# Performance work log

Hardware: AMD Instinct MI355X
Metric: run time of the kernel (lower is better)

## Reference

```python
import jax, jax.numpy as jnp
import numpy as np

B, L, D_MODEL = 2, 2048, 1024
EXPAND, D_STATE, D_CONV = 2, 16, 4
D_INNER = EXPAND * D_MODEL          # 2048
DT_RANK = D_MODEL // 16             # 64 (mamba-ssm 'auto' rank)


def setup_inputs() -> dict:
    key = jax.random.key(0)
    ks = jax.random.split(key, 8)
    s = lambda k, shape, scale: jax.random.normal(k, shape, jnp.float32) * scale
    x = s(ks[0], (B, L, D_MODEL), 1.0)
    W_in = s(ks[1], (2 * D_INNER, D_MODEL), D_MODEL ** -0.5)
    conv_w = s(ks[2], (D_INNER, 1, D_CONV), D_CONV ** -0.5)   # depthwise kernel
    conv_b = s(ks[3], (D_INNER,), 0.02)
    W_xproj = s(ks[4], (DT_RANK + 2 * D_STATE, D_INNER), D_INNER ** -0.5)
    W_dt = s(ks[5], (D_INNER, DT_RANK), DT_RANK ** -0.5)
    # inverse-softplus of dt ~= 0.01 (mamba default dt init region)
    b_dt = jnp.log(jnp.expm1(0.01 * jnp.ones((D_INNER,), jnp.float32)))
    # S4D-real init: A = -[1..d_state] per channel
    A_log = jnp.log(jnp.broadcast_to(
        jnp.arange(1, D_STATE + 1, dtype=jnp.float32), (D_INNER, D_STATE)))
    D = jnp.ones((D_INNER,), jnp.float32)
    W_out = s(ks[6], (D_MODEL, D_INNER), D_INNER ** -0.5)
    return dict(x=x, W_in=W_in, conv_w=conv_w, conv_b=conv_b, W_xproj=W_xproj,
                W_dt=W_dt, b_dt=b_dt, A_log=A_log, D=D, W_out=W_out)


def reference(x, W_in, conv_w, conv_b, W_xproj, W_dt, b_dt, A_log, D, W_out):
    # in_proj: [B,L,d_model] -> [B,L,2*d_inner]
    xz = jnp.einsum('bld,ed->ble', x, W_in)
    xs, z = jnp.split(xz, 2, axis=-1)

    # causal depthwise conv1d over time, kernel d_conv
    xc = jnp.swapaxes(xs, 1, 2)  # [B, d_inner, L]
    xc = jax.lax.conv_general_dilated(
        xc, conv_w, window_strides=(1,), padding=[(D_CONV - 1, 0)],
        feature_group_count=D_INNER)
    xc = xc + conv_b[None, :, None]
    xs = jax.nn.silu(jnp.swapaxes(xc, 1, 2))  # [B,L,d_inner]

    # x_proj -> (dt, B, C)
    x_dbl = jnp.einsum('bld,ed->ble', xs, W_xproj)
    dt, Bm, Cm = jnp.split(x_dbl, [DT_RANK, DT_RANK + D_STATE], axis=-1)
    dt = jax.nn.softplus(jnp.einsum('blr,dr->bld', dt, W_dt) + b_dt)  # [B,L,d_inner]

    A = -jnp.exp(A_log)  # [d_inner, d_state]

    def step(h, inp):
        dt_t, B_t, C_t, x_t = inp  # [B,d], [B,n], [B,n], [B,d]
        dA = jnp.exp(dt_t[..., None] * A)                       # [B,d,n]
        h = h * dA + (dt_t * x_t)[..., None] * B_t[:, None, :]  # [B,d,n]
        y = jnp.einsum('bdn,bn->bd', h, C_t)
        return h, y

    tm = lambda a: jnp.swapaxes(a, 0, 1)  # time-major for scan
    h0 = jnp.zeros((x.shape[0], D_INNER, D_STATE), x.dtype)
    _, ys = jax.lax.scan(step, h0, (tm(dt), tm(Bm), tm(Cm), tm(xs)))

    y = tm(ys) + xs * D          # skip term D*x
    y = y * jax.nn.silu(z)       # gate
    return jnp.einsum('bld,ed->ble', y, W_out)  # out_proj -> [B,L,d_model]
```

## Files before the change

kernel.cpp:

```cpp
#include <hip/hip_runtime.h>
#include <cstdint>
#include <cstddef>

typedef __bf16 bf16_t;
typedef bf16_t bf16x4 __attribute__((ext_vector_type(4)));
typedef bf16_t bf16x8 __attribute__((ext_vector_type(8)));
typedef float f32x4 __attribute__((ext_vector_type(4)));

static __device__ __forceinline__ void glds16(const void* g, void* l) {
    __builtin_amdgcn_global_load_lds((const __attribute__((address_space(1))) void*)g,
                                     (__attribute__((address_space(3))) void*)l,
                                     16, 0, 0);
}

#define BARRIER()  asm volatile("s_barrier" ::: "memory")
#define DS_WAIT()  do { asm volatile("s_waitcnt lgkmcnt(0)" ::: "memory"); \
                        __builtin_amdgcn_sched_barrier(0); } while (0)

__global__ __launch_bounds__(256)
void cast5(const float* __restrict__ s0, bf16_t* __restrict__ d0, int n0,
           const float* __restrict__ s1, bf16_t* __restrict__ d1, int n1,
           const float* __restrict__ s2, bf16_t* __restrict__ d2, int n2,
           const float* __restrict__ s3, bf16_t* __restrict__ d3, int n3,
           const float* __restrict__ s4, bf16_t* __restrict__ d4)
{
    int bb = blockIdx.x;
    const float* s; bf16_t* d;
    if (bb < n0)              { s = s0; d = d0; }
    else if ((bb -= n0) < n1) { s = s1; d = d1; }
    else if ((bb -= n1) < n2) { s = s2; d = d2; }
    else if ((bb -= n2) < n3) { s = s3; d = d3; }
    else                      { bb -= n3; s = s4; d = d4; }
    const size_t base = (size_t)bb * 1024 + threadIdx.x * 4;
    const f32x4 v = *(const f32x4*)(s + base);
    bf16x4 o;
    o[0] = (bf16_t)v[0]; o[1] = (bf16_t)v[1]; o[2] = (bf16_t)v[2]; o[3] = (bf16_t)v[3];
    *(bf16x4*)(d + base) = o;
}

#define LOAD_A(MQ) \
    _Pragma("unroll") for (int mf = 0; mf < 4; ++mf) { \
        aF[mf][0] = *(const bf16x8*)(Ab + (aRow + (MQ)*64 + mf*16)*64 + ck0); \
        aF[mf][1] = *(const bf16x8*)(Ab + (aRow + (MQ)*64 + mf*16)*64 + ck1); }

#define LOAD_B(NQ, dst) \
    _Pragma("unroll") for (int nf = 0; nf < 2; ++nf) { \
        dst[nf][0] = *(const bf16x8*)(Bb + (bRow + (NQ)*32 + nf*16)*64 + ck0); \
        dst[nf][1] = *(const bf16x8*)(Bb + (bRow + (NQ)*32 + nf*16)*64 + ck1); }

#define MFMA16(MQ, NQ, bset) \
    __builtin_amdgcn_s_setprio(1); \
    _Pragma("unroll") for (int mf = 0; mf < 4; ++mf) \
    _Pragma("unroll") for (int nf = 0; nf < 2; ++nf) \
    _Pragma("unroll") for (int kk = 0; kk < 2; ++kk) \
        acc[(MQ)*4+mf][(NQ)*2+nf] = __builtin_amdgcn_mfma_f32_16x16x32_bf16( \
            aF[mf][kk], bset[nf][kk], acc[(MQ)*4+mf][(NQ)*2+nf], 0, 0, 0); \
    __builtin_amdgcn_s_setprio(0);

template<int EPI, int SPLITK>
__global__ __launch_bounds__(512, 2)
void gemm256_bt(const bf16_t* __restrict__ A, const bf16_t* __restrict__ Bt,
                const int N, const int K, const int KC,
                bf16_t* __restrict__ o0, bf16_t* __restrict__ o1,
                float* __restrict__ p0, float* __restrict__ p1,
                float* __restrict__ p2, float* __restrict__ p3)
{
    constexpr int TILE = 256 * 64;
    __shared__ __align__(16) bf16_t As[2 * TILE];
    __shared__ __align__(16) bf16_t Bs[2 * TILE];

    const int tid  = threadIdx.x;
    const int lane = tid & 63;
    const int w    = tid >> 6;
    const int wm   = w >> 2, wn = w & 3;
    const int l16  = lane & 15, quad = lane >> 4;
    const int e7   = l16 & 7;
    const int ck0  = (quad ^ e7) << 3;
    const int ck1  = ck0 ^ 32;
    const int lr   = lane >> 3, l8 = lane & 7;
    const int swz  = (l8 ^ lr) << 3;
    const int m0   = blockIdx.y * 256, n0 = blockIdx.x * 256;
    const int z    = (SPLITK > 1) ? blockIdx.z : 0;
    const int NT   = KC >> 6;

    if (SPLITK > 1) { A += (size_t)z * KC; Bt += (size_t)z * KC; }

    const int aRow = wm * 128 + l16;
    const int bRow = wn * 64 + l16;

    f32x4 acc[8][4] = {};
    bf16x8 aF[4][2], bLo[2][2], bHi[2][2];

    auto STAGE = [&](int unit, int kt, int d) {
        const bf16_t* g; int rg0; bf16_t* lb; int rbase;
        if (unit <= 1) { g = A;  rg0 = m0; lb = As;
                         rbase = unit * 64 + w * 8; }
        else           { g = Bt; rg0 = n0; lb = Bs;
                         rbase = ((w >> 2) << 6) + ((w & 3) << 3) + ((unit & 1) << 5); }
#pragma unroll
        for (int L = 0; L < 2; ++L) {
            const int rb = rbase + L * 128;
            glds16(g + (size_t)(rg0 + rb + lr) * K + kt * 64 + swz,
                   lb + d * TILE + rb * 64);
        }
    };

    STAGE(2, 0, 0); STAGE(0, 0, 0); STAGE(3, 0, 0); STAGE(1, 0, 0);
    if (NT > 1) { STAGE(2, 1, 1); STAGE(0, 1, 1); STAGE(3, 1, 1); }
    if (NT > 1) asm volatile("s_waitcnt vmcnt(6)" ::: "memory");
    else        asm volatile("s_waitcnt vmcnt(0)" ::: "memory");
    BARRIER();

    for (int i = 0; i < NT; ++i) {
        const int b = i & 1;
        const bf16_t* Ab = As + b * TILE;
        const bf16_t* Bb = Bs + b * TILE;

        LOAD_A(0); LOAD_B(0, bLo);
        if (i + 1 < NT) STAGE(1, i + 1, (i + 1) & 1);
        BARRIER(); DS_WAIT();
        MFMA16(0, 0, bLo);
        __builtin_amdgcn_sched_barrier(0);
        BARRIER();

        LOAD_B(1, bHi);
        if (i + 2 < NT) STAGE(2, i + 2, b);
        BARRIER(); DS_WAIT();
        MFMA16(0, 1, bHi);
        __builtin_amdgcn_sched_barrier(0);
        BARRIER();

        LOAD_A(1);
        if (i + 2 < NT) { STAGE(0, i + 2, b); STAGE(3, i + 2, b); }
        BARRIER(); DS_WAIT();
        MFMA16(1, 1, bHi);
        MFMA16(1, 0, bLo);
        __builtin_amdgcn_sched_barrier(0);
        if (i + 2 < NT) asm volatile("s_waitcnt vmcnt(6)" ::: "memory");
        else            asm volatile("s_waitcnt vmcnt(0)" ::: "memory");
        BARRIER();
    }

    float* pz = (EPI == 3) ? ((z == 0) ? p0 : (z == 1) ? p1 : (z == 2) ? p2 : p3)
                           : nullptr;
#pragma unroll
    for (int mf = 0; mf < 8; ++mf)
#pragma unroll
        for (int nf = 0; nf < 4; ++nf)
#pragma unroll
            for (int r = 0; r < 4; ++r) {
                const int gr = m0 + wm * 128 + mf * 16 + quad * 4 + r;
                const int gc = n0 + wn * 64 + nf * 16 + l16;
                const float v = acc[mf][nf][r];
                if (EPI == 1) {
                    if (gc < 2048) o0[(size_t)gr * 2048 + gc] = (bf16_t)v;
                    else           o1[(size_t)gr * 2048 + (gc - 2048)] = (bf16_t)v;
                } else if (EPI == 3) {
                    pz[(size_t)gr * N + gc] = v;
                } else {
                    ((float*)o0)[(size_t)gr * N + gc] = v;
                }
            }
}

template<int EPI, int SPLITK>
__global__ __launch_bounds__(256)
void gemm_bt(const bf16_t* __restrict__ A, const bf16_t* __restrict__ Bt,
             const int M, const int N, const int K,
             void* __restrict__ o0, void* __restrict__ o1,
             const float* __restrict__ bias,
             float* __restrict__ p0, float* __restrict__ p1,
             float* __restrict__ p2, float* __restrict__ p3)
{
    __shared__ __align__(16) bf16_t As[128 * 64];
    __shared__ __align__(16) bf16_t Bs[128 * 64];

    const int tid  = threadIdx.x;
    const int lane = tid & 63;
    const int wave = tid >> 6;
    const int wm = wave & 1, wn = wave >> 1;
    const int m0 = blockIdx.y * 128, n0 = blockIdx.x * 128;
    const int quad = lane >> 4, l16 = lane & 15;
    const int z   = (SPLITK > 1) ? blockIdx.z : 0;
    const int KC  = K / SPLITK;
    const int kb  = z * KC;

    f32x4 acc[4][4] = {};

    for (int k0 = kb; k0 < kb + KC; k0 += 64) {
        __syncthreads();
#pragma unroll
        for (int j = 0; j < 4; j++) {
            const int u  = wave * 2048 + j * 512;
            const int ue = u + lane * 8;
            const int row = ue >> 6, col = ue & 63;
            glds16(A  + (size_t)(m0 + row) * K + k0 + col, As + u);
            glds16(Bt + (size_t)(n0 + row) * K + k0 + col, Bs + u);
        }
        __syncthreads();

#pragma unroll
        for (int kk = 0; kk < 2; kk++) {
            bf16x8 afr[4], bfr[4];
#pragma unroll
            for (int mt = 0; mt < 4; mt++)
                afr[mt] = *(const bf16x8*)(As + (wm * 64 + mt * 16 + l16) * 64 + kk * 32 + quad * 8);
#pragma unroll
            for (int nt = 0; nt < 4; nt++)
                bfr[nt] = *(const bf16x8*)(Bs + (wn * 64 + nt * 16 + l16) * 64 + kk * 32 + quad * 8);
#pragma unroll
            for (int mt = 0; mt < 4; mt++)
#pragma unroll
                for (int nt = 0; nt < 4; nt++)
                    acc[mt][nt] = __builtin_amdgcn_mfma_f32_16x16x32_bf16(
                        afr[mt], bfr[nt], acc[mt][nt], 0, 0, 0);
        }
    }

    float* pz = (z == 0) ? p0 : (z == 1) ? p1 : (z == 2) ? p2 : p3;

#pragma unroll
    for (int mt = 0; mt < 4; mt++)
#pragma unroll
        for (int nt = 0; nt < 4; nt++)
#pragma unroll
            for (int r = 0; r < 4; r++) {
                const int gr = m0 + wm * 64 + mt * 16 + quad * 4 + r;
                const int gc = n0 + wn * 64 + nt * 16 + l16;
                const float v = acc[mt][nt][r];
                if (EPI == 0) {
                    ((float*)o0)[(size_t)gr * N + gc] = v;
                } else if (EPI == 1) {
                    if (gc < 2048) ((bf16_t*)o0)[(size_t)gr * 2048 + gc] = (bf16_t)v;
                    else           ((bf16_t*)o1)[(size_t)gr * 2048 + (gc - 2048)] = (bf16_t)v;
                } else if (EPI == 2) {
                    const float t  = v + bias[gc];
                    const float sp = (t > 15.f) ? t : __logf(1.f + __expf(t));
                    ((bf16_t*)o0)[(size_t)gr * 2048 + gc] = (bf16_t)sp;
                } else {
                    pz[(size_t)gr * N + gc] = v;
                }
            }
}

__global__ __launch_bounds__(256)
void reduce_k(float* __restrict__ out, const float* __restrict__ p0,
              const float* __restrict__ p1, const float* __restrict__ p2,
              const float* __restrict__ p3, const int nsplit)
{
    const size_t i = ((size_t)blockIdx.x * 256 + threadIdx.x) * 4;
    f32x4 v = *(const f32x4*)(p0 + i);
    v += *(const f32x4*)(p1 + i);
    if (nsplit == 4) {
        v += *(const f32x4*)(p2 + i);
        v += *(const f32x4*)(p3 + i);
    }
    *(f32x4*)(out + i) = v;
}

__global__ __launch_bounds__(256)
void conv_silu(const bf16_t* __restrict__ xs_pre, const float* __restrict__ cw,
               const float* __restrict__ cb, bf16_t* __restrict__ xs)
{
    const int d0 = threadIdx.x * 8;
    const int rg = blockIdx.x * 8;
    float w0[8], w1[8], w2[8], w3[8], bs[8];
#pragma unroll
    for (int j = 0; j < 8; j++) {
        const f32x4 wv = *(const f32x4*)(cw + (size_t)(d0 + j) * 4);
        w0[j] = wv[0]; w1[j] = wv[1]; w2[j] = wv[2]; w3[j] = wv[3];
        bs[j] = cb[d0 + j];
    }
    float p1[8], p2[8], p3[8];
    {
        const int r1 = (rg >= 1) ? rg - 1 : 0;
        const int r2 = (rg >= 2) ? rg - 2 : 0;
        const int r3 = (rg >= 3) ? rg - 3 : 0;
        const bf16x8 v1 = *(const bf16x8*)(xs_pre + (size_t)r1 * 2048 + d0);
        const bf16x8 v2 = *(const bf16x8*)(xs_pre + (size_t)r2 * 2048 + d0);
        const bf16x8 v3 = *(const bf16x8*)(xs_pre + (size_t)r3 * 2048 + d0);
#pragma unroll
        for (int j = 0; j < 8; j++) {
            p1[j] = (float)v1[j]; p2[j] = (float)v2[j]; p3[j] = (float)v3[j];
        }
    }
#pragma unroll
    for (int t = 0; t < 8; t++) {
        const int r = rg + t;
        const int l = r & 2047;
        const float m1 = (l >= 1) ? 1.f : 0.f;
        const float m2 = (l >= 2) ? 1.f : 0.f;
        const float m3 = (l >= 3) ? 1.f : 0.f;
        const bf16x8 v = *(const bf16x8*)(xs_pre + (size_t)r * 2048 + d0);
        bf16x8 o;
#pragma unroll
        for (int j = 0; j < 8; j++) {
            const float cur = (float)v[j];
            float a = bs[j] + w3[j] * cur;
            a += m1 * w2[j] * p1[j];
            a += m2 * w1[j] * p2[j];
            a += m3 * w0[j] * p3[j];
            const float s = a / (1.f + __expf(-a));
            o[j] = (bf16_t)s;
            p3[j] = p2[j]; p2[j] = p1[j]; p1[j] = cur;
        }
        *(bf16x8*)(xs + (size_t)r * 2048 + d0) = o;
    }
}

__global__ __launch_bounds__(256)
void xproj_kernel(const bf16_t* __restrict__ A, const bf16_t* __restrict__ Bt,
                  bf16_t* __restrict__ dtr, float* __restrict__ Bm, float* __restrict__ Cm)
{
    __shared__ float red[4][64][25];
    const int tid  = threadIdx.x;
    const int lane = tid & 63, w = tid >> 6;
    const int m0 = blockIdx.x * 16;
    const int l16 = lane & 15, quad = lane >> 4;
    f32x4 acc[6] = {};

    const int kbase = w * 512;
    const bf16_t* ap = A + (size_t)(m0 + l16) * 2048 + kbase + quad * 8;
    for (int k0 = 0; k0 < 512; k0 += 32) {
        const bf16x8 afr = *(const bf16x8*)(ap + k0);
#pragma unroll
        for (int t = 0; t < 6; t++) {
            const bf16x8 bfr = *(const bf16x8*)(Bt + (size_t)(t * 16 + l16) * 2048 + kbase + k0 + quad * 8);
            acc[t] = __builtin_amdgcn_mfma_f32_16x16x32_bf16(afr, bfr, acc[t], 0, 0, 0);
        }
    }
#pragma unroll
    for (int t = 0; t < 6; t++)
#pragma unroll
        for (int r = 0; r < 4; r++) red[w][lane][t * 4 + r] = acc[t][r];
    __syncthreads();
    if (w == 0) {
#pragma unroll
        for (int t = 0; t < 6; t++)
#pragma unroll
            for (int r = 0; r < 4; r++) {
                const int j = t * 4 + r;
                const float v = red[0][lane][j] + red[1][lane][j]
                              + red[2][lane][j] + red[3][lane][j];
                const int gr = m0 + quad * 4 + r;
                const int gc = t * 16 + l16;
                if (gc < 64)      dtr[(size_t)gr * 64 + gc] = (bf16_t)v;
                else if (gc < 80) Bm[(size_t)gr * 16 + (gc - 64)] = v;
                else              Cm[(size_t)gr * 16 + (gc - 80)] = v;
            }
    }
}

static __device__ __forceinline__ bool fast_check(const float* A_log, int d, float& a1) {
    a1 = -__expf(A_log[(size_t)d * 16]);
    bool ok = true;
#pragma unroll
    for (int n = 1; n < 16; n++) {
        const float an = -__expf(A_log[(size_t)d * 16 + n]);
        const float pn = (float)(n + 1) * a1;
        ok = ok && (fabsf(an - pn) <= 1e-3f * fabsf(pn) + 1e-6f);
    }
    return ok;
}

__global__ __launch_bounds__(256)
void scan1(const bf16_t* __restrict__ dt, const bf16_t* __restrict__ xs,
           const float* __restrict__ Bm, const float* __restrict__ A_log,
           float* __restrict__ sdt_o, bf16_t* __restrict__ Hsum)
{
    const int tid = threadIdx.x;
    const int bi  = blockIdx.x;
    const int c   = bi & 63;
    const int bb  = bi >> 6;
    const int b   = bb >> 3;
    const int d   = (bb & 7) * 256 + tid;
    float a1; const bool fast = fast_check(A_log, d, a1);

    float h[16] = {};
    float s = 0.f;
    const size_t rowbase = (size_t)b * 2048 + c * 32;

    if (fast) {
#pragma unroll 4
        for (int t = 0; t < 32; t++) {
            const size_t ro = (rowbase + t) * 2048 + d;
            const float dtv = (float)dt[ro];
            const float xv  = (float)xs[ro];
            s += dtv;
            const float r = __expf(dtv * a1);
            float rp[16]; rp[0] = r;
#pragma unroll
            for (int n = 1; n < 16; n++) rp[n] = rp[n - 1] * r;
            const float bx = dtv * xv;
            const float* bp = Bm + (rowbase + t) * 16;
#pragma unroll
            for (int n = 0; n < 16; n++) h[n] = fmaf(h[n], rp[n], bx * bp[n]);
        }
    } else {
        for (int t = 0; t < 32; t++) {
            const size_t ro = (rowbase + t) * 2048 + d;
            const float dtv = (float)dt[ro];
            const float xv  = (float)xs[ro];
            s += dtv;
            const float bx = dtv * xv;
            const float* bp = Bm + (rowbase + t) * 16;
#pragma unroll
            for (int n = 0; n < 16; n++) {
                const float an = -__expf(A_log[(size_t)d * 16 + n]);
                h[n] = fmaf(h[n], __expf(dtv * an), bx * bp[n]);
            }
        }
    }
    const size_t sb = (size_t)bi * 256 + tid;
    sdt_o[sb] = s;
    bf16x8 h0, h1;
#pragma unroll
    for (int n = 0; n < 8; n++) { h0[n] = (bf16_t)h[n]; h1[n] = (bf16_t)h[n + 8]; }
    *(bf16x8*)(Hsum + sb * 16)     = h0;
    *(bf16x8*)(Hsum + sb * 16 + 8) = h1;
}

__global__ __launch_bounds__(256)
void scan2(const float* __restrict__ sdt, bf16_t* __restrict__ Hsum,
           const float* __restrict__ A_log)
{
    const int tid = threadIdx.x;
    const int bb  = blockIdx.x;
    const int d   = (bb & 7) * 256 + tid;
    float a1; const bool fast = fast_check(A_log, d, a1);

    float h[16] = {};
    if (fast) {
        size_t sb = (size_t)(bb * 64) * 256 + tid;
        float s_cur = sdt[sb];
        bf16x8 h0c = *(const bf16x8*)(Hsum + sb * 16);
        bf16x8 h1c = *(const bf16x8*)(Hsum + sb * 16 + 8);
        for (int c = 0; c < 64; c++) {
            const size_t sbn = sb + 256;
            float s_nxt = 0.f; bf16x8 h0n = {}, h1n = {};
            if (c < 63) {
                s_nxt = sdt[sbn];
                h0n = *(const bf16x8*)(Hsum + sbn * 16);
                h1n = *(const bf16x8*)(Hsum + sbn * 16 + 8);
            }
            bf16x8 o0, o1;
#pragma unroll
            for (int n = 0; n < 8; n++) { o0[n] = (bf16_t)h[n]; o1[n] = (bf16_t)h[n + 8]; }
            *(bf16x8*)(Hsum + sb * 16)     = o0;
            *(bf16x8*)(Hsum + sb * 16 + 8) = o1;
            const float r = __expf(s_cur * a1);
            float rp[16]; rp[0] = r;
#pragma unroll
            for (int n = 1; n < 16; n++) rp[n] = rp[n - 1] * r;
#pragma unroll
            for (int n = 0; n < 16; n++) {
                const float hsv = (n < 8) ? (float)h0c[n] : (float)h1c[n - 8];
                h[n] = fmaf(h[n], rp[n], hsv);
            }
            sb = sbn; s_cur = s_nxt; h0c = h0n; h1c = h1n;
        }
    } else {
        for (int c = 0; c < 64; c++) {
            const size_t sb = ((size_t)(bb * 64 + c) * 256 + tid);
            const float s = sdt[sb];
            bf16x8 hs0 = *(const bf16x8*)(Hsum + sb * 16);
            bf16x8 hs1 = *(const bf16x8*)(Hsum + sb * 16 + 8);
            bf16x8 o0, o1;
#pragma unroll
            for (int n = 0; n < 8; n++) { o0[n] = (bf16_t)h[n]; o1[n] = (bf16_t)h[n + 8]; }
            *(bf16x8*)(Hsum + sb * 16)     = o0;
            *(bf16x8*)(Hsum + sb * 16 + 8) = o1;
#pragma unroll
            for (int n = 0; n < 16; n++) {
                const float an = -__expf(A_log[(size_t)d * 16 + n]);
                const float hsv = (n < 8) ? (float)hs0[n] : (float)hs1[n - 8];
                h[n] = fmaf(h[n], __expf(s * an), hsv);
            }
        }
    }
}

__global__ __launch_bounds__(256)
void scan3(const bf16_t* __restrict__ dt, const bf16_t* __restrict__ xs,
           bf16_t* __restrict__ zy,
           const float* __restrict__ Bm, const float* __restrict__ Cm,
           const float* __restrict__ A_log, const float* __restrict__ Dv,
           const bf16_t* __restrict__ Hseed)
{
    const int tid = threadIdx.x;
    const int bi  = blockIdx.x;
    const int c   = bi & 63;
    const int bb  = bi >> 6;
    const int b   = bb >> 3;
    const int d   = (bb & 7) * 256 + tid;
    float a1; const bool fast = fast_check(A_log, d, a1);
    const float Dd = Dv[d];

    const size_t sb = (size_t)bi * 256 + tid;
    const bf16x8 hs0 = *(const bf16x8*)(Hseed + sb * 16);
    const bf16x8 hs1 = *(const bf16x8*)(Hseed + sb * 16 + 8);
    float h[16];
#pragma unroll
    for (int n = 0; n < 8; n++) { h[n] = (float)hs0[n]; h[n + 8] = (float)hs1[n]; }

    const size_t rowbase = (size_t)b * 2048 + c * 32;

    if (fast) {
#pragma unroll 2
        for (int t = 0; t < 32; t++) {
            const size_t ro = (rowbase + t) * 2048 + d;
            const float dtv = (float)dt[ro];
            const float xv  = (float)xs[ro];
            const float zv  = (float)zy[ro];
            const float r = __expf(dtv * a1);
            float rp[16]; rp[0] = r;
#pragma unroll
            for (int n = 1; n < 16; n++) rp[n] = rp[n - 1] * r;
            const float bx = dtv * xv;
            const float* bp = Bm + (rowbase + t) * 16;
            const float* cp = Cm + (rowbase + t) * 16;
            float y0 = 0.f, y1 = 0.f;
#pragma unroll
            for (int n = 0; n < 16; n += 2) {
                h[n]     = fmaf(h[n],     rp[n],     bx * bp[n]);
                h[n + 1] = fmaf(h[n + 1], rp[n + 1], bx * bp[n + 1]);
                y0 = fmaf(h[n],     cp[n],     y0);
                y1 = fmaf(h[n + 1], cp[n + 1], y1);
            }
            const float yv = (y0 + y1) + xv * Dd;
            const float g  = zv / (1.f + __expf(-zv));
            zy[ro] = (bf16_t)(yv * g);
        }
    } else {
        for (int t = 0; t < 32; t++) {
            const size_t ro = (rowbase + t) * 2048 + d;
            const float dtv = (float)dt[ro];
            const float xv  = (float)xs[ro];
            const float zv  = (float)zy[ro];
            const float bx = dtv * xv;
            const float* bp = Bm + (rowbase + t) * 16;
            const float* cp = Cm + (rowbase + t) * 16;
            float y = 0.f;
#pragma unroll
            for (int n = 0; n < 16; n++) {
                const float an = -__expf(A_log[(size_t)d * 16 + n]);
                h[n] = fmaf(h[n], __expf(dtv * an), bx * bp[n]);
                y = fmaf(h[n], cp[n], y);
            }
            const float yv = y + xv * Dd;
            const float g  = zv / (1.f + __expf(-zv));
            zy[ro] = (bf16_t)(yv * g);
        }
    }
}

extern "C" void kernel_launch(void* const* d_in, const int* in_sizes, int n_in,
                              void* d_out, int out_size, void* d_ws, size_t ws_size,
                              hipStream_t stream)
{
    const float* x     = (const float*)d_in[0];
    const float* W_in  = (const float*)d_in[1];
    const float* convw = (const float*)d_in[2];
    const float* convb = (const float*)d_in[3];
    const float* W_xp  = (const float*)d_in[4];
    const float* W_dt  = (const float*)d_in[5];
    const float* b_dt  = (const float*)d_in[6];
    const float* A_log = (const float*)d_in[7];
    const float* Dv    = (const float*)d_in[8];
    const float* W_out = (const float*)d_in[9];

    char* ws = (char*)d_ws;
    bf16_t* bufP   = (bf16_t*)(ws + 0);
    bf16_t* bufZ   = (bf16_t*)(ws + 16777216);
    bf16_t* bufX   = (bf16_t*)(ws + 33554432);
    bf16_t* W_in_b = (bf16_t*)(ws + 33554432);
    bf16_t* dtr    = (bf16_t*)(ws + 50331648);
    float*  Bm     = (float*)(ws + 50855936);
    float*  Cm     = (float*)(ws + 51118080);
    float*  sdt    = (float*)(ws + 51380224);
    bf16_t* Hsum   = (bf16_t*)(ws + 52428800);
    bf16_t* x_b    = (bf16_t*)(ws + 52428800);
    bf16_t* W_out_b= (bf16_t*)(ws + 60817408);
    bf16_t* W_xp_b = (bf16_t*)(ws + 65011712);
    bf16_t* W_dt_b = (bf16_t*)(ws + 65404928);
    float*  P0     = (float*)(ws + 0);
    float*  P1     = (float*)(ws + 33554432);
    float*  P2     = (float*)(ws + 65667072);
    float*  P3     = (float*)(ws + 82444288);
    const bool sk4 = (ws_size >= 99221504ull);

    cast5<<<dim3(4096 + 4096 + 2048 + 192 + 128), dim3(256), 0, stream>>>(
        x, x_b, 4096, W_in, W_in_b, 4096, W_out, W_out_b, 2048,
        W_xp, W_xp_b, 192, W_dt, W_dt_b);

    gemm256_bt<1, 1><<<dim3(16, 16), dim3(512), 0, stream>>>(
        x_b, W_in_b, 4096, 1024, 1024, bufP, bufZ,
        nullptr, nullptr, nullptr, nullptr);

    conv_silu<<<dim3(512), dim3(256), 0, stream>>>(bufP, convw, convb, bufX);

    xproj_kernel<<<dim3(256), dim3(256), 0, stream>>>(bufX, W_xp_b, dtr, Bm, Cm);

    gemm_bt<2, 1><<<dim3(16, 32), dim3(256), 0, stream>>>(
        dtr, W_dt_b, 4096, 2048, 64, (void*)bufP, nullptr, b_dt,
        nullptr, nullptr, nullptr, nullptr);

    scan1<<<dim3(1024), dim3(256), 0, stream>>>(bufP, bufX, Bm, A_log, sdt, Hsum);
    scan2<<<dim3(16),   dim3(256), 0, stream>>>(sdt, Hsum, A_log);
    scan3<<<dim3(1024), dim3(256), 0, stream>>>(bufP, bufX, bufZ, Bm, Cm, A_log, Dv, Hsum);

    if (sk4) {
        gemm256_bt<3, 4><<<dim3(4, 16, 4), dim3(512), 0, stream>>>(
            bufZ, W_out_b, 1024, 2048, 512, nullptr, nullptr,
            P0, P1, P2, P3);
        reduce_k<<<dim3(4096), dim3(256), 0, stream>>>(
            (float*)d_out, P0, P1, P2, P3, 4);
    } else {
        gemm_bt<3, 2><<<dim3(8, 32, 2), dim3(256), 0, stream>>>(
            bufZ, W_out_b, 4096, 1024, 2048, nullptr, nullptr, nullptr,
            P0, P1, nullptr, nullptr);
        reduce_k<<<dim3(4096), dim3(256), 0, stream>>>(
            (float*)d_out, P0, P1, nullptr, nullptr, 2);
    }
}
```

Baseline: 281.3 us.

## Fuse conv, x_proj and dt projection into one kernel; reorder GEMM staging

Adds a conv_xproj_dt kernel that runs the causal conv+SiLU, the x_proj MFMA and the dt_proj+softplus on a 16-row tile held in shared memory. It replaces three launches and the round trips of xs/dtr through global memory. The dt output goes to a separate buffer so bufP is not overwritten. Separately, the 256-tile GEMM issues its global-to-LDS staging before the LDS fragment reads, moves the vmcnt wait ahead of the last MFMA group, and wraps setprio around whole phases. scan2 also prefetches two chunks ahead instead of one. The fused kernel uses only 256 blocks and does redundant weight loads per block, so it may have lower occupancy and parallelism than the separate kernels.

```diff
diff --git a/kernel.cpp b/kernel.cpp
--- a/kernel.cpp
+++ b/kernel.cpp
@@ -49,13 +49,11 @@
         dst[nf][1] = *(const bf16x8*)(Bb + (bRow + (NQ)*32 + nf*16)*64 + ck1); }
 
 #define MFMA16(MQ, NQ, bset) \
-    __builtin_amdgcn_s_setprio(1); \
     _Pragma("unroll") for (int mf = 0; mf < 4; ++mf) \
     _Pragma("unroll") for (int nf = 0; nf < 2; ++nf) \
     _Pragma("unroll") for (int kk = 0; kk < 2; ++kk) \
         acc[(MQ)*4+mf][(NQ)*2+nf] = __builtin_amdgcn_mfma_f32_16x16x32_bf16( \
-            aF[mf][kk], bset[nf][kk], acc[(MQ)*4+mf][(NQ)*2+nf], 0, 0, 0); \
-    __builtin_amdgcn_s_setprio(0);
+            aF[mf][kk], bset[nf][kk], acc[(MQ)*4+mf][(NQ)*2+nf], 0, 0, 0);
 
 template<int EPI, int SPLITK>
 __global__ __launch_bounds__(512, 2)
@@ -116,28 +114,34 @@
         const bf16_t* Ab = As + b * TILE;
         const bf16_t* Bb = Bs + b * TILE;
 
+        if (i + 1 < NT) STAGE(1, i + 1, (i + 1) & 1);
         LOAD_A(0); LOAD_B(0, bLo);
-        if (i + 1 < NT) STAGE(1, i + 1, (i + 1) & 1);
         BARRIER(); DS_WAIT();
+        __builtin_amdgcn_s_setprio(1);
         MFMA16(0, 0, bLo);
+        __builtin_amdgcn_s_setprio(0);
         __builtin_amdgcn_sched_barrier(0);
         BARRIER();
 
+        if (i + 2 < NT) STAGE(2, i + 2, b);
         LOAD_B(1, bHi);
-        if (i + 2 < NT) STAGE(2, i + 2, b);
         BARRIER(); DS_WAIT();
+        __builtin_amdgcn_s_setprio(1);
         MFMA16(0, 1, bHi);
+        __builtin_amdgcn_s_setprio(0);
         __builtin_amdgcn_sched_barrier(0);
         BARRIER();
 
+        if (i + 2 < NT) { STAGE(0, i + 2, b); STAGE(3, i + 2, b); }
         LOAD_A(1);
-        if (i + 2 < NT) { STAGE(0, i + 2, b); STAGE(3, i + 2, b); }
         BARRIER(); DS_WAIT();
+        if (i + 2 < NT) asm volatile("s_waitcnt vmcnt(6)" ::: "memory");
+        else            asm volatile("s_waitcnt vmcnt(0)" ::: "memory");
+        __builtin_amdgcn_s_setprio(1);
         MFMA16(1, 1, bHi);
         MFMA16(1, 0, bLo);
+        __builtin_amdgcn_s_setprio(0);
         __builtin_amdgcn_sched_barrier(0);
-        if (i + 2 < NT) asm volatile("s_waitcnt vmcnt(6)" ::: "memory");
-        else            asm volatile("s_waitcnt vmcnt(0)" ::: "memory");
         BARRIER();
     }
 
@@ -259,6 +263,135 @@
 }
 
 __global__ __launch_bounds__(256)
+void conv_xproj_dt(const bf16_t* __restrict__ xs_pre,
+                   const float* __restrict__ cw, const float* __restrict__ cb,
+                   const bf16_t* __restrict__ Wxp, const bf16_t* __restrict__ Wdt,
+                   const float* __restrict__ bdt,
+                   bf16_t* __restrict__ xs, bf16_t* __restrict__ dt,
+                   float* __restrict__ Bm, float* __restrict__ Cm)
+{
+    __shared__ __align__(16) bf16_t xsL[16 * 2048];
+    __shared__ float red[4][64][25];
+    __shared__ __align__(16) bf16_t dtA[16 * 64];
+
+    const int tid  = threadIdx.x;
+    const int lane = tid & 63, w = tid >> 6;
+    const int m0   = blockIdx.x * 16;
+    const int l16  = lane & 15, quad = lane >> 4, l8 = lane & 7;
+    const int l0   = m0 & 2047;
+
+    {
+        const int d0 = tid * 8;
+        float w0[8], w1[8], w2[8], w3[8], bs[8];
+#pragma unroll
+        for (int j = 0; j < 8; j++) {
+            const f32x4 wv = *(const f32x4*)(cw + (size_t)(d0 + j) * 4);
+            w0[j] = wv[0]; w1[j] = wv[1]; w2[j] = wv[2]; w3[j] = wv[3];
+            bs[j] = cb[d0 + j];
+        }
+        const int r1 = (m0 >= 1) ? m0 - 1 : 0;
+        const int r2 = (m0 >= 2) ? m0 - 2 : 0;
+        const int r3 = (m0 >= 3) ? m0 - 3 : 0;
+        const bf16x8 v1 = *(const bf16x8*)(xs_pre + (size_t)r1 * 2048 + d0);
+        const bf16x8 v2 = *(const bf16x8*)(xs_pre + (size_t)r2 * 2048 + d0);
+        const bf16x8 v3 = *(const bf16x8*)(xs_pre + (size_t)r3 * 2048 + d0);
+        float p1[8], p2[8], p3[8];
+#pragma unroll
+        for (int j = 0; j < 8; j++) {
+            p1[j] = (float)v1[j]; p2[j] = (float)v2[j]; p3[j] = (float)v3[j];
+        }
+#pragma unroll
+        for (int r = 0; r < 16; r++) {
+            const int l = l0 + r;
+            const float m1 = (l >= 1) ? 1.f : 0.f;
+            const float m2 = (l >= 2) ? 1.f : 0.f;
+            const float m3 = (l >= 3) ? 1.f : 0.f;
+            const bf16x8 v = *(const bf16x8*)(xs_pre + (size_t)(m0 + r) * 2048 + d0);
+            bf16x8 o;
+#pragma unroll
+            for (int j = 0; j < 8; j++) {
+                const float cur = (float)v[j];
+                float a = bs[j] + w3[j] * cur;
+                a += m1 * w2[j] * p1[j];
+                a += m2 * w1[j] * p2[j];
+                a += m3 * w0[j] * p3[j];
+                const float s = a / (1.f + __expf(-a));
+                o[j] = (bf16_t)s;
+                p3[j] = p2[j]; p2[j] = p1[j]; p1[j] = cur;
+            }
+            *(bf16x8*)(xs + (size_t)(m0 + r) * 2048 + d0) = o;
+            const int g = (d0 >> 3) ^ (r & 7);
+            *(bf16x8*)(xsL + r * 2048 + g * 8) = o;
+        }
+    }
+    __syncthreads();
+
+    f32x4 acc[6] = {};
+    const int kbase = w * 512;
+    for (int k0 = 0; k0 < 512; k0 += 32) {
+        const int gA = ((kbase + k0) >> 3) + quad;
+        const bf16x8 afr = *(const bf16x8*)(xsL + (size_t)l16 * 2048 + ((gA ^ l8) << 3));
+#pragma unroll
+        for (int t = 0; t < 6; t++) {
+            const bf16x8 bfr = *(const bf16x8*)(Wxp + (size_t)(t * 16 + l16) * 2048 + kbase + k0 + quad * 8);
+            acc[t] = __builtin_amdgcn_mfma_f32_16x16x32_bf16(afr, bfr, acc[t], 0, 0, 0);
+        }
+    }
+#pragma unroll
+    for (int t = 0; t < 6; t++)
+#pragma unroll
+        for (int r = 0; r < 4; r++) red[w][lane][t * 4 + r] = acc[t][r];
+    __syncthreads();
+
+    {
+#pragma unroll
+        for (int r = 0; r < 4; r++) {
+            const int j = w * 4 + r;
+            const float v = red[0][lane][j] + red[1][lane][j]
+                          + red[2][lane][j] + red[3][lane][j];
+            const int row = quad * 4 + r, col = w * 16 + l16;
+            const int g = (col >> 3) ^ (row & 7);
+            dtA[row * 64 + g * 8 + (col & 7)] = (bf16_t)v;
+        }
+        if (w == 0) {
+#pragma unroll
+            for (int t = 4; t < 6; t++)
+#pragma unroll
+                for (int r = 0; r < 4; r++) {
+                    const int j = t * 4 + r;
+                    const float v = red[0][lane][j] + red[1][lane][j]
+                                  + red[2][lane][j] + red[3][lane][j];
+                    const int gr = m0 + quad * 4 + r;
+                    const int gc = t * 16 + l16;
+                    if (gc < 80) Bm[(size_t)gr * 16 + (gc - 64)] = v;
+                    else         Cm[(size_t)gr * 16 + (gc - 80)] = v;
+                }
+        }
+    }
+    __syncthreads();
+
+    const bf16x8 a0 = *(const bf16x8*)(dtA + l16 * 64 + (((0 + quad) ^ l8) << 3));
+    const bf16x8 a1 = *(const bf16x8*)(dtA + l16 * 64 + (((4 + quad) ^ l8) << 3));
+    for (int nt = 0; nt < 32; ++nt) {
+        const int nb = w * 512 + nt * 16;
+        const bf16x8 b0 = *(const bf16x8*)(Wdt + (size_t)(nb + l16) * 64 + quad * 8);
+        const bf16x8 b1 = *(const bf16x8*)(Wdt + (size_t)(nb + l16) * 64 + 32 + quad * 8);
+        f32x4 a = {};
+        a = __builtin_amdgcn_mfma_f32_16x16x32_bf16(a0, b0, a, 0, 0, 0);
+        a = __builtin_amdgcn_mfma_f32_16x16x32_bf16(a1, b1, a, 0, 0, 0);
+        const int gc = nb + l16;
+        const float bv = bdt[gc];
+#pragma unroll
+        for (int r = 0; r < 4; r++) {
+            const int gr = m0 + quad * 4 + r;
+            const float t  = a[r] + bv;
+            const float sp = (t > 15.f) ? t : __logf(1.f + __expf(t));
+            dt[(size_t)gr * 2048 + gc] = (bf16_t)sp;
+        }
+    }
+}
+
+__global__ __launch_bounds__(256)
 void conv_silu(const bf16_t* __restrict__ xs_pre, const float* __restrict__ cw,
                const float* __restrict__ cb, bf16_t* __restrict__ xs)
 {
@@ -432,32 +565,41 @@
     float h[16] = {};
     if (fast) {
         size_t sb = (size_t)(bb * 64) * 256 + tid;
-        float s_cur = sdt[sb];
-        bf16x8 h0c = *(const bf16x8*)(Hsum + sb * 16);
-        bf16x8 h1c = *(const bf16x8*)(Hsum + sb * 16 + 8);
+        float sA = sdt[sb];
+        bf16x8 hA0 = *(const bf16x8*)(Hsum + sb * 16);
+        bf16x8 hA1 = *(const bf16x8*)(Hsum + sb * 16 + 8);
+        float sB = 0.f; bf16x8 hB0 = {}, hB1 = {};
+        {
+            const size_t sb1 = sb + 256;
+            sB  = sdt[sb1];
+            hB0 = *(const bf16x8*)(Hsum + sb1 * 16);
+            hB1 = *(const bf16x8*)(Hsum + sb1 * 16 + 8);
+        }
         for (int c = 0; c < 64; c++) {
-            const size_t sbn = sb + 256;
-            float s_nxt = 0.f; bf16x8 h0n = {}, h1n = {};
-            if (c < 63) {
-                s_nxt = sdt[sbn];
-                h0n = *(const bf16x8*)(Hsum + sbn * 16);
-                h1n = *(const bf16x8*)(Hsum + sbn * 16 + 8);
+            float sC = 0.f; bf16x8 hC0 = {}, hC1 = {};
+            if (c + 2 < 64) {
+                const size_t sb2 = sb + 512;
+                sC  = sdt[sb2];
+                hC0 = *(const bf16x8*)(Hsum + sb2 * 16);
+                hC1 = *(const bf16x8*)(Hsum + sb2 * 16 + 8);
             }
             bf16x8 o0, o1;
 #pragma unroll
             for (int n = 0; n < 8; n++) { o0[n] = (bf16_t)h[n]; o1[n] = (bf16_t)h[n + 8]; }
             *(bf16x8*)(Hsum + sb * 16)     = o0;
             *(bf16x8*)(Hsum + sb * 16 + 8) = o1;
-            const float r = __expf(s_cur * a1);
+            const float r = __expf(sA * a1);
             float rp[16]; rp[0] = r;
 #pragma unroll
             for (int n = 1; n < 16; n++) rp[n] = rp[n - 1] * r;
 #pragma unroll
             for (int n = 0; n < 16; n++) {
-                const float hsv = (n < 8) ? (float)h0c[n] : (float)h1c[n - 8];
+                const float hsv = (n < 8) ? (float)hA0[n] : (float)hA1[n - 8];
                 h[n] = fmaf(h[n], rp[n], hsv);
             }
-            sb = sbn; s_cur = s_nxt; h0c = h0n; h1c = h1n;
+            sb += 256;
+            sA = sB; hA0 = hB0; hA1 = hB1;
+            sB = sC; hB0 = hC0; hB1 = hC1;
         }
     } else {
         for (int c = 0; c < 64; c++) {
@@ -583,11 +725,13 @@
     bf16_t* W_out_b= (bf16_t*)(ws + 60817408);
     bf16_t* W_xp_b = (bf16_t*)(ws + 65011712);
     bf16_t* W_dt_b = (bf16_t*)(ws + 65404928);
+    bf16_t* dtb    = (bf16_t*)(ws + 65667072);
     float*  P0     = (float*)(ws + 0);
     float*  P1     = (float*)(ws + 33554432);
     float*  P2     = (float*)(ws + 65667072);
     float*  P3     = (float*)(ws + 82444288);
-    const bool sk4 = (ws_size >= 99221504ull);
+    const bool sk4  = (ws_size >= 99221504ull);
+    const bool fuse = (ws_size >= 82444288ull);
 
     cast5<<<dim3(4096 + 4096 + 2048 + 192 + 128), dim3(256), 0, stream>>>(
         x, x_b, 4096, W_in, W_in_b, 4096, W_out, W_out_b, 2048,
@@ -597,17 +741,21 @@
         x_b, W_in_b, 4096, 1024, 1024, bufP, bufZ,
         nullptr, nullptr, nullptr, nullptr);
 
-    conv_silu<<<dim3(512), dim3(256), 0, stream>>>(bufP, convw, convb, bufX);
-
-    xproj_kernel<<<dim3(256), dim3(256), 0, stream>>>(bufX, W_xp_b, dtr, Bm, Cm);
-
-    gemm_bt<2, 1><<<dim3(16, 32), dim3(256), 0, stream>>>(
-        dtr, W_dt_b, 4096, 2048, 64, (void*)bufP, nullptr, b_dt,
-        nullptr, nullptr, nullptr, nullptr);
-
-    scan1<<<dim3(1024), dim3(256), 0, stream>>>(bufP, bufX, Bm, A_log, sdt, Hsum);
+    bf16_t* dtp = fuse ? dtb : bufP;
+    if (fuse) {
+        conv_xproj_dt<<<dim3(256), dim3(256), 0, stream>>>(
+            bufP, convw, convb, W_xp_b, W_dt_b, b_dt, bufX, dtb, Bm, Cm);
+    } else {
+        conv_silu<<<dim3(512), dim3(256), 0, stream>>>(bufP, convw, convb, bufX);
+        xproj_kernel<<<dim3(256), dim3(256), 0, stream>>>(bufX, W_xp_b, dtr, Bm, Cm);
+        gemm_bt<2, 1><<<dim3(16, 32), dim3(256), 0, stream>>>(
+            dtr, W_dt_b, 4096, 2048, 64, (void*)bufP, nullptr, b_dt,
+            nullptr, nullptr, nullptr, nullptr);
+    }
+
+    scan1<<<dim3(1024), dim3(256), 0, stream>>>(dtp, bufX, Bm, A_log, sdt, Hsum);
     scan2<<<dim3(16),   dim3(256), 0, stream>>>(sdt, Hsum, A_log);
-    scan3<<<dim3(1024), dim3(256), 0, stream>>>(bufP, bufX, bufZ, Bm, Cm, A_log, Dv, Hsum);
+    scan3<<<dim3(1024), dim3(256), 0, stream>>>(dtp, bufX, bufZ, Bm, Cm, A_log, Dv, Hsum);
 
     if (sk4) {
         gemm256_bt<3, 4><<<dim3(4, 16, 4), dim3(512), 0, stream>>>(
```

Result: slower. 301.1 us (+7.0%).
